# Optimization experiments

Hardware: AMD Instinct MI355X
Metric: run time of the kernel (lower is better)

Reference implementation:

```python
import jax, jax.numpy as jnp
import numpy as np

N_NODES = 100000
N_EDGES = 300000
N_GRAPHS = 2048
F_ATOM = 40
D_IN = 128    # GINInputSize
D_HID = 256   # GINHiddenSize
D_OUT = 512   # FPSize
D_TASK = 1    # OutputSize


def _glorot(key, shape):
    fan_in, fan_out = shape[0], shape[1]
    lim = (6.0 / (fan_in + fan_out)) ** 0.5
    return jax.random.uniform(key, shape, jnp.float32, -lim, lim)


def setup_inputs() -> dict:
    key = jax.random.key(0)
    ks = jax.random.split(key, 16)
    inp = {
        'x': jax.random.normal(ks[0], (N_NODES, F_ATOM), jnp.float32),
        'edge_index': jax.random.randint(ks[1], (2, N_EDGES), 0, N_NODES, jnp.int64),
        'batch': jnp.sort(jax.random.randint(ks[2], (N_NODES,), 0, N_GRAPHS, jnp.int64)),
        # NodeFeatEmbed: MLP([F_ATOM, D_IN]) == single Linear (plain_last)
        'W_embed': _glorot(ks[3], (F_ATOM, D_IN)),
        'b_embed': jnp.zeros((D_IN,), jnp.float32),
        # GINConv eps per layer (train_eps=False -> 0.0 constants)
        'eps': jnp.zeros((3,), jnp.float32),
        # layer 0: MLP([D_IN, D_HID, D_HID])
        'W1_0': _glorot(ks[4], (D_IN, D_HID)),  'b1_0': jnp.zeros((D_HID,), jnp.float32),
        'W2_0': _glorot(ks[5], (D_HID, D_HID)), 'b2_0': jnp.zeros((D_HID,), jnp.float32),
        # layer 1: MLP([D_HID, D_HID, D_HID])
        'W1_1': _glorot(ks[6], (D_HID, D_HID)), 'b1_1': jnp.zeros((D_HID,), jnp.float32),
        'W2_1': _glorot(ks[7], (D_HID, D_HID)), 'b2_1': jnp.zeros((D_HID,), jnp.float32),
        # layer 2 (last, maps to out_channels=FPSize): MLP([D_HID, D_OUT, D_OUT])
        'W1_2': _glorot(ks[8], (D_HID, D_OUT)), 'b1_2': jnp.zeros((D_OUT,), jnp.float32),
        'W2_2': _glorot(ks[9], (D_OUT, D_OUT)), 'b2_2': jnp.zeros((D_OUT,), jnp.float32),
        # task head
        'W_task': _glorot(ks[10], (D_OUT, D_TASK)),
        'b_task': jnp.zeros((D_TASK,), jnp.float32),
    }
    return inp


def _gin_forward(x, edge_index, batch, W_embed, b_embed, eps, layers, W_task, b_task):
    src, dst = edge_index[0], edge_index[1]
    # NodeFeatEmbed
    h = x @ W_embed + b_embed                                    # [N, D_IN]
    n_layers = len(layers)
    for l, (W1, b1, W2, b2) in enumerate(layers):
        # GINConv: MLP((1+eps)*h + sum_{j->i} h_j)
        agg = jax.ops.segment_sum(h[src], dst, num_segments=N_NODES)
        z = (1.0 + eps[l]) * h + agg
        h = jax.nn.relu(z @ W1 + b1) @ W2 + b2
        if l < n_layers - 1:                                     # inter-layer act (not after last)
            h = jax.nn.relu(h)
    # global_add_pool readout
    pooled = jax.ops.segment_sum(h, batch, num_segments=N_GRAPHS)  # [G, D_OUT]
    return pooled @ W_task + b_task                               # [G, D_TASK]


def reference(x, edge_index, batch, W_embed, b_embed, eps,
              W1_0, b1_0, W2_0, b2_0,
              W1_1, b1_1, W2_1, b2_1,
              W1_2, b1_2, W2_2, b2_2,
              W_task, b_task):
    layers = [(W1_0, b1_0, W2_0, b2_0), (W1_1, b1_1, W2_1, b2_1), (W1_2, b1_2, W2_2, b2_2)]
    return _gin_forward(x, edge_index, batch, W_embed, b_embed, eps, layers, W_task, b_task)
```

## Files before the change

### kernel.cpp

```cpp
#include <hip/hip_runtime.h>

#define N_NODES 100000
#define E_EDGES 300000
#define N_GRAPHS 2048

typedef float  floatx4 __attribute__((ext_vector_type(4)));
typedef short  shortx8 __attribute__((ext_vector_type(8)));

__device__ __forceinline__ float bf2f(unsigned short u) {
  return __uint_as_float(((unsigned int)u) << 16);
}
__device__ __forceinline__ unsigned short f2bf(float f) {
  unsigned int u = __float_as_uint(f);
  u += 0x7FFFu + ((u >> 16) & 1u);
  return (unsigned short)(u >> 16);
}

__device__ __forceinline__ void cp16(const void* g, void* l) {
  __builtin_amdgcn_global_load_lds(
      (const __attribute__((address_space(1))) unsigned int*)g,
      (__attribute__((address_space(3))) unsigned int*)l, 16, 0, 0);
}

struct WtJobs {
  const float* W[4];
  unsigned short* Wt[4];
  int K[4];
  int N[4];
};

__global__ __launch_bounds__(256)
void wt4_kernel(WtJobs j) {
  __shared__ unsigned short tile[32][33];
  const int z = blockIdx.z;
  const int K = j.K[z], N = j.N[z];
  const int kb = blockIdx.x * 32, nb = blockIdx.y * 32;
  if (kb >= K || nb >= N) return;
  const float* W = j.W[z];
  unsigned short* Wt = j.Wt[z];
  const int tx = threadIdx.x & 31, ty = threadIdx.x >> 5;
  for (int r = ty; r < 32; r += 8)
    tile[r][tx] = f2bf(W[(size_t)(kb + r) * N + nb + tx]);
  __syncthreads();
  for (int r = ty; r < 32; r += 8)
    Wt[(size_t)(nb + r) * K + kb + tx] = tile[tx][r];
}

__global__ __launch_bounds__(256)
void wf_kernel(const float* __restrict__ We, const float* __restrict__ be,
               const float* __restrict__ W1, unsigned short* __restrict__ WfT) {
  const int n = threadIdx.x;
  const int k = blockIdx.x;
  if (k < 40) {
    float s = 0.f;
    for (int j = 0; j < 128; j++) s = fmaf(We[k * 128 + j], W1[(size_t)j * 256 + n], s);
    WfT[n * 64 + k] = f2bf(s);
  } else {
    float s = 0.f;
    for (int j = 0; j < 128; j++) s = fmaf(be[j], W1[(size_t)j * 256 + n], s);
    WfT[n * 64 + 40] = f2bf(s);
    for (int kk = 41; kk < 64; kk++) WfT[n * 64 + kk] = 0;
  }
}

__global__ __launch_bounds__(256)
void w2v_kernel(const float* __restrict__ W2, const float* __restrict__ b2,
                const float* __restrict__ wt, float* __restrict__ w2v,
                float* __restrict__ c2) {
  const int lane = threadIdx.x & 63;
  const int wave = threadIdx.x >> 6;
  if (blockIdx.x < 128) {
    const int k = blockIdx.x * 4 + wave;
    const float* row = W2 + (size_t)k * 512 + lane * 8;
    float4 a0 = *(const float4*)(row);
    float4 a1 = *(const float4*)(row + 4);
    float4 w0 = *(const float4*)(wt + lane * 8);
    float4 w1 = *(const float4*)(wt + lane * 8 + 4);
    float s = a0.x * w0.x + a0.y * w0.y + a0.z * w0.z + a0.w * w0.w +
              a1.x * w1.x + a1.y * w1.y + a1.z * w1.z + a1.w * w1.w;
#pragma unroll
    for (int off = 32; off > 0; off >>= 1) s += __shfl_down(s, off);
    if (lane == 0) w2v[k] = s;
  } else if (wave == 0) {
    float4 a0 = *(const float4*)(b2 + lane * 8);
    float4 a1 = *(const float4*)(b2 + lane * 8 + 4);
    float4 w0 = *(const float4*)(wt + lane * 8);
    float4 w1 = *(const float4*)(wt + lane * 8 + 4);
    float s = a0.x * w0.x + a0.y * w0.y + a0.z * w0.z + a0.w * w0.w +
              a1.x * w1.x + a1.y * w1.y + a1.z * w1.z + a1.w * w1.w;
#pragma unroll
    for (int off = 32; off > 0; off >>= 1) s += __shfl_down(s, off);
    if (lane == 0) *c2 = s;
  }
}

__global__ __launch_bounds__(256)
void init_nd_kernel(float* __restrict__ nd, const float* __restrict__ c2) {
  int i = blockIdx.x * 256 + threadIdx.x;
  if (i < N_NODES) nd[i] = *c2;
}

__global__ __launch_bounds__(256)
void zero_kernel(int* __restrict__ p, int n) {
  int i = blockIdx.x * 256 + threadIdx.x;
  if (i < n) p[i] = 0;
}

__global__ __launch_bounds__(256)
void hist_kernel(const int* __restrict__ ei, int* __restrict__ deg) {
  int e = blockIdx.x * 256 + threadIdx.x;
  if (e < E_EDGES) atomicAdd(&deg[ei[E_EDGES + e]], 1);
}

__global__ __launch_bounds__(256)
void scan_blk_kernel(const int* __restrict__ in, int* __restrict__ out,
                     int* __restrict__ blk_sums, int n_in, int n_out) {
  __shared__ int sm[256];
  const int t = threadIdx.x;
  const int base = blockIdx.x * 1024 + t * 4;
  int d0 = (base + 0 < n_in) ? in[base + 0] : 0;
  int d1 = (base + 1 < n_in) ? in[base + 1] : 0;
  int d2 = (base + 2 < n_in) ? in[base + 2] : 0;
  int d3 = (base + 3 < n_in) ? in[base + 3] : 0;
  int s = d0 + d1 + d2 + d3;
  sm[t] = s;
  __syncthreads();
  for (int off = 1; off < 256; off <<= 1) {
    int v = (t >= off) ? sm[t - off] : 0;
    __syncthreads();
    sm[t] += v;
    __syncthreads();
  }
  int excl = sm[t] - s;
  if (base + 0 < n_out) out[base + 0] = excl;
  if (base + 1 < n_out) out[base + 1] = excl + d0;
  if (base + 2 < n_out) out[base + 2] = excl + d0 + d1;
  if (base + 3 < n_out) out[base + 3] = excl + d0 + d1 + d2;
  if (t == 255 && blk_sums) blk_sums[blockIdx.x] = sm[255];
}

__global__ __launch_bounds__(256)
void scan_fix_kernel(int* __restrict__ row_ptr, const int* __restrict__ blk_off,
                     int* __restrict__ cursor) {
  int i = blockIdx.x * 256 + threadIdx.x;
  if (i <= N_NODES) {
    int v = row_ptr[i] + blk_off[i >> 10];
    row_ptr[i] = v;
    if (i < N_NODES) cursor[i] = v;
  }
}

__global__ __launch_bounds__(256)
void fill_kernel(const int* __restrict__ ei, int* __restrict__ cursor,
                 int* __restrict__ csr_src) {
  int e = blockIdx.x * 256 + threadIdx.x;
  if (e < E_EDGES) {
    int d = ei[E_EDGES + e];
    int slot = atomicAdd(&cursor[d], 1);
    csr_src[slot] = ei[e];
  }
}

__global__ __launch_bounds__(256)
void gatherx_kernel(const float* __restrict__ X, unsigned short* __restrict__ G,
                    const int* __restrict__ row_ptr, const int* __restrict__ csr,
                    const float* __restrict__ eps) {
  const int node = blockIdx.x * 4 + (threadIdx.x >> 6);
  const int lane = threadIdx.x & 63;
  const float sc = 1.0f + eps[0];
  const int e0 = row_ptr[node];
  const int e1 = row_ptr[node + 1];
  float acc = 0.f;
  if (lane < 40) {
    acc = sc * X[(size_t)node * 40 + lane];
    int e = e0;
    for (; e + 4 <= e1; e += 4) {
      int s0 = csr[e], s1 = csr[e + 1], s2 = csr[e + 2], s3 = csr[e + 3];
      float a0 = X[(size_t)s0 * 40 + lane];
      float a1 = X[(size_t)s1 * 40 + lane];
      float a2 = X[(size_t)s2 * 40 + lane];
      float a3 = X[(size_t)s3 * 40 + lane];
      acc += (a0 + a1) + (a2 + a3);
    }
    for (; e < e1; e++)
      acc += X[(size_t)csr[e] * 40 + lane];
  } else if (lane == 40) {
    acc = sc + (float)(e1 - e0);
  }
  G[(size_t)node * 64 + lane] = f2bf(acc);
}

__global__ __launch_bounds__(256)
void gather_kernel(const unsigned short* __restrict__ H, unsigned short* __restrict__ Z,
                   const int* __restrict__ row_ptr, const int* __restrict__ csr,
                   const float* __restrict__ eps, int l) {
  const int node = blockIdx.x * 4 + (threadIdx.x >> 6);
  const int lane = threadIdx.x & 63;
  const float sc = 1.0f + eps[l];
  uint2 hv = *(const uint2*)(H + (size_t)node * 256 + lane * 4);
  float acc[4];
  acc[0] = sc * bf2f((unsigned short)(hv.x & 0xFFFF));
  acc[1] = sc * bf2f((unsigned short)(hv.x >> 16));
  acc[2] = sc * bf2f((unsigned short)(hv.y & 0xFFFF));
  acc[3] = sc * bf2f((unsigned short)(hv.y >> 16));
  const int e0 = row_ptr[node];
  const int e1 = row_ptr[node + 1];
  int e = e0;
  for (; e + 4 <= e1; e += 4) {
    int s0 = csr[e], s1 = csr[e + 1], s2 = csr[e + 2], s3 = csr[e + 3];
    uint2 a = *(const uint2*)(H + (size_t)s0 * 256 + lane * 4);
    uint2 b = *(const uint2*)(H + (size_t)s1 * 256 + lane * 4);
    uint2 c = *(const uint2*)(H + (size_t)s2 * 256 + lane * 4);
    uint2 d = *(const uint2*)(H + (size_t)s3 * 256 + lane * 4);
    acc[0] += (bf2f((unsigned short)(a.x & 0xFFFF)) + bf2f((unsigned short)(b.x & 0xFFFF))) +
              (bf2f((unsigned short)(c.x & 0xFFFF)) + bf2f((unsigned short)(d.x & 0xFFFF)));
    acc[1] += (bf2f((unsigned short)(a.x >> 16)) + bf2f((unsigned short)(b.x >> 16))) +
              (bf2f((unsigned short)(c.x >> 16)) + bf2f((unsigned short)(d.x >> 16)));
    acc[2] += (bf2f((unsigned short)(a.y & 0xFFFF)) + bf2f((unsigned short)(b.y & 0xFFFF))) +
              (bf2f((unsigned short)(c.y & 0xFFFF)) + bf2f((unsigned short)(d.y & 0xFFFF)));
    acc[3] += (bf2f((unsigned short)(a.y >> 16)) + bf2f((unsigned short)(b.y >> 16))) +
              (bf2f((unsigned short)(c.y >> 16)) + bf2f((unsigned short)(d.y >> 16)));
  }
  for (; e < e1; e++) {
    int s0 = csr[e];
    uint2 a = *(const uint2*)(H + (size_t)s0 * 256 + lane * 4);
    acc[0] += bf2f((unsigned short)(a.x & 0xFFFF));
    acc[1] += bf2f((unsigned short)(a.x >> 16));
    acc[2] += bf2f((unsigned short)(a.y & 0xFFFF));
    acc[3] += bf2f((unsigned short)(a.y >> 16));
  }
  unsigned short z[4] = {f2bf(acc[0]), f2bf(acc[1]), f2bf(acc[2]), f2bf(acc[3])};
  *(uint2*)(Z + (size_t)node * 256 + lane * 4) = *(uint2*)z;
}

template <int K, int NXL, int MODE>
__global__ __launch_bounds__(256, 4)
void gemm_kernel(const unsigned short* __restrict__ A,
                 const unsigned short* __restrict__ Bt,
                 const float* __restrict__ bias, unsigned short* __restrict__ C,
                 const float* __restrict__ w2v, float* __restrict__ nodedot,
                 int M, int N) {
  const int g = blockIdx.x;
  const int mblk = ((g >> (3 + NXL)) << 3) | (g & 7);
  const int nblk = (g >> 3) & ((1 << NXL) - 1);
  const int m0 = mblk * 128;
  const int n0 = nblk * 128;
  if (m0 >= M) return;

  __shared__ unsigned short smem[2 * 128 * 64];
  unsigned short* As = smem;
  unsigned short* Bs = smem + 128 * 64;
  const int tid = threadIdx.x;
  const int lane = tid & 63;
  const int wave = tid >> 6;
  const int wm = (wave & 1) * 64;
  const int wn = (wave >> 1) * 64;
  const int fr = lane & 15;
  const int fq = lane >> 4;

  floatx4 acc[4][4];
#pragma unroll
  for (int i = 0; i < 4; i++)
#pragma unroll
    for (int j = 0; j < 4; j++) acc[i][j] = (floatx4){0.f, 0.f, 0.f, 0.f};

  const unsigned short* gA[4];
  const unsigned short* gB[4];
  unsigned short* lA[4];
  unsigned short* lB[4];
#pragma unroll
  for (int p = 0; p < 4; p++) {
    int c = p * 256 + wave * 64 + lane;
    int row = c >> 3;
    int q = (c & 7) ^ (row & 7);
    int grA = m0 + row;
    if (grA >= M) grA = M - 1;
    gA[p] = A + (size_t)grA * K + q * 8;
    gB[p] = Bt + (size_t)(n0 + row) * K + q * 8;
    lA[p] = &As[(p * 256 + wave * 64) * 8];
    lB[p] = &Bs[(p * 256 + wave * 64) * 8];
  }

  for (int k0 = 0; k0 < K; k0 += 64) {
#pragma unroll
    for (int p = 0; p < 4; p++) cp16(gA[p] + k0, lA[p]);
#pragma unroll
    for (int p = 0; p < 4; p++) cp16(gB[p] + k0, lB[p]);
    __syncthreads();
#pragma unroll
    for (int s0 = 0; s0 < 2; s0++) {
      shortx8 af[4], bf[4];
#pragma unroll
      for (int i = 0; i < 4; i++)
        af[i] = *(const shortx8*)&As[(wm + i * 16 + fr) * 64 +
                                     (((s0 * 4 + fq) ^ (fr & 7)) * 8)];
#pragma unroll
      for (int j = 0; j < 4; j++)
        bf[j] = *(const shortx8*)&Bs[(wn + j * 16 + fr) * 64 +
                                     (((s0 * 4 + fq) ^ (fr & 7)) * 8)];
#pragma unroll
      for (int i = 0; i < 4; i++)
#pragma unroll
        for (int j = 0; j < 4; j++)
          acc[i][j] = __builtin_amdgcn_mfma_f32_16x16x32_bf16(af[i], bf[j], acc[i][j], 0, 0, 0);
    }
    __syncthreads();
  }

  if (MODE == 3) {
    float wv[4], bj[4];
#pragma unroll
    for (int j = 0; j < 4; j++) {
      int col = n0 + wn + j * 16 + fr;
      wv[j] = w2v[col];
      bj[j] = bias[col];
    }
#pragma unroll
    for (int i = 0; i < 4; i++) {
#pragma unroll
      for (int r = 0; r < 4; r++) {
        float p = 0.f;
#pragma unroll
        for (int j = 0; j < 4; j++) p += fmaxf(acc[i][j][r] + bj[j], 0.f) * wv[j];
#pragma unroll
        for (int off = 1; off < 16; off <<= 1) p += __shfl_xor(p, off);
        if (fr == 0) {
          int row = m0 + wm + i * 16 + fq * 4 + r;
          if (row < M) unsafeAtomicAdd(&nodedot[row], p);
        }
      }
    }
  } else {
    unsigned short* Cs = smem;
#pragma unroll
    for (int j = 0; j < 4; j++) {
      int col = wn + j * 16 + fr;
      float bj = bias[n0 + col];
#pragma unroll
      for (int i = 0; i < 4; i++) {
#pragma unroll
        for (int r = 0; r < 4; r++) {
          int row = wm + i * 16 + fq * 4 + r;
          Cs[row * 128 + col] = f2bf(fmaxf(acc[i][j][r] + bj, 0.f));
        }
      }
    }
    __syncthreads();
    const int rcol = (tid & 15) * 8;
#pragma unroll
    for (int p = 0; p < 8; p++) {
      int row = p * 16 + (tid >> 4);
      int grow = m0 + row;
      if (grow < M) {
        uint4 v = *(const uint4*)&Cs[row * 128 + rcol];
        *(uint4*)&C[(size_t)grow * N + n0 + rcol] = v;
      }
    }
  }
}

__global__ __launch_bounds__(256)
void init_out_kernel(float* __restrict__ out, const float* __restrict__ b_task) {
  int g = blockIdx.x * 256 + threadIdx.x;
  if (g < N_GRAPHS) out[g] = b_task[0];
}

__global__ __launch_bounds__(256)
void pool_kernel(const float* __restrict__ nodedot, const int* __restrict__ batch,
                 float* __restrict__ out) {
  int t = blockIdx.x * 256 + threadIdx.x;
  int i0 = t * 64;
  if (i0 >= N_NODES) return;
  int i1 = i0 + 64;
  if (i1 > N_NODES) i1 = N_NODES;
  int g = batch[i0];
  float s = 0.f;
  for (int i = i0; i < i1; i++) {
    int gi = batch[i];
    if (gi != g) { unsafeAtomicAdd(&out[g], s); g = gi; s = 0.f; }
    s += nodedot[i];
  }
  unsafeAtomicAdd(&out[g], s);
}

extern "C" void kernel_launch(void* const* d_in, const int* in_sizes, int n_in,
                              void* d_out, int out_size, void* d_ws, size_t ws_size,
                              hipStream_t stream) {
  const float* x       = (const float*)d_in[0];
  const int*   ei      = (const int*)d_in[1];
  const int*   batch   = (const int*)d_in[2];
  const float* W_embed = (const float*)d_in[3];
  const float* b_embed = (const float*)d_in[4];
  const float* eps     = (const float*)d_in[5];
  const float* W1[3] = {(const float*)d_in[6],  (const float*)d_in[10], (const float*)d_in[14]};
  const float* B1[3] = {(const float*)d_in[7],  (const float*)d_in[11], (const float*)d_in[15]};
  const float* W2[3] = {(const float*)d_in[8],  (const float*)d_in[12], (const float*)d_in[16]};
  const float* B2[3] = {(const float*)d_in[9],  (const float*)d_in[13], (const float*)d_in[17]};
  const float* W_task = (const float*)d_in[18];
  const float* b_task = (const float*)d_in[19];
  float* out = (float*)d_out;

  const size_t OFF_RB  = 51200000;
  const size_t OFF_RZ  = 102400000;
  const size_t OFF_AUX = 153600000;
  if (ws_size < OFF_AUX + 4000000) return;
  unsigned short* RH = (unsigned short*)d_ws;
  unsigned short* RB = (unsigned short*)((char*)d_ws + OFF_RB);
  unsigned short* RZ = (unsigned short*)((char*)d_ws + OFF_RZ);
  char* aux = (char*)d_ws + OFF_AUX;
  int* row_ptr  = (int*)(aux);
  int* cursor   = (int*)(aux + 400016);
  int* csr_src  = (int*)(aux + 800016);
  int* blk_sums = (int*)(aux + 2000016);
  int* blk_off  = (int*)(aux + 2000416);
  float* nodedot = (float*)(aux + 2000816);
  unsigned short* WT = (unsigned short*)(aux + 2400832);
  float* w2v = (float*)(aux + 3200832);
  float* c2  = (float*)(aux + 3202880);
  unsigned short* WfT    = WT;
  unsigned short* Wt2_0  = WT + 32768;
  unsigned short* Wt1_1  = WT + 98304;
  unsigned short* Wt2_1  = WT + 163840;
  unsigned short* Wt1_2  = WT + 229376;

  WtJobs jobs;
  jobs.W[0] = W2[0]; jobs.Wt[0] = Wt2_0; jobs.K[0] = 256; jobs.N[0] = 256;
  jobs.W[1] = W1[1]; jobs.Wt[1] = Wt1_1; jobs.K[1] = 256; jobs.N[1] = 256;
  jobs.W[2] = W2[1]; jobs.Wt[2] = Wt2_1; jobs.K[2] = 256; jobs.N[2] = 256;
  jobs.W[3] = W1[2]; jobs.Wt[3] = Wt1_2; jobs.K[3] = 256; jobs.N[3] = 512;
  wt4_kernel<<<dim3(8, 16, 4), 256, 0, stream>>>(jobs);

  wf_kernel<<<41, 256, 0, stream>>>(W_embed, b_embed, W1[0], WfT);
  w2v_kernel<<<129, 256, 0, stream>>>(W2[2], B2[2], W_task, w2v, c2);

  zero_kernel<<<(N_NODES + 255) / 256, 256, 0, stream>>>(cursor, N_NODES);
  hist_kernel<<<(E_EDGES + 255) / 256, 256, 0, stream>>>(ei, cursor);
  scan_blk_kernel<<<98, 256, 0, stream>>>(cursor, row_ptr, blk_sums, N_NODES, N_NODES + 1);
  scan_blk_kernel<<<1, 256, 0, stream>>>(blk_sums, blk_off, nullptr, 98, 98);
  scan_fix_kernel<<<(N_NODES + 256) / 256, 256, 0, stream>>>(row_ptr, blk_off, cursor);
  fill_kernel<<<(E_EDGES + 255) / 256, 256, 0, stream>>>(ei, cursor, csr_src);

  init_nd_kernel<<<(N_NODES + 255) / 256, 256, 0, stream>>>(nodedot, c2);

  const int MB = (N_NODES + 127) / 128;
  const int MB8 = ((MB + 7) / 8) * 8;

  gatherx_kernel<<<N_NODES / 4, 256, 0, stream>>>(x, RZ, row_ptr, csr_src, eps);
  gemm_kernel<64, 1, 0><<<2 * MB8, 256, 0, stream>>>(RZ, WfT, B1[0], RB, nullptr, nullptr, N_NODES, 256);
  gemm_kernel<256, 1, 0><<<2 * MB8, 256, 0, stream>>>(RB, Wt2_0, B2[0], RH, nullptr, nullptr, N_NODES, 256);

  gather_kernel<<<N_NODES / 4, 256, 0, stream>>>(RH, RZ, row_ptr, csr_src, eps, 1);
  gemm_kernel<256, 1, 0><<<2 * MB8, 256, 0, stream>>>(RZ, Wt1_1, B1[1], RB, nullptr, nullptr, N_NODES, 256);
  gemm_kernel<256, 1, 0><<<2 * MB8, 256, 0, stream>>>(RB, Wt2_1, B2[1], RH, nullptr, nullptr, N_NODES, 256);

  gather_kernel<<<N_NODES / 4, 256, 0, stream>>>(RH, RZ, row_ptr, csr_src, eps, 2);
  gemm_kernel<256, 2, 3><<<4 * MB8, 256, 0, stream>>>(RZ, Wt1_2, B1[2], nullptr, w2v, nodedot, N_NODES, 512);

  init_out_kernel<<<(N_GRAPHS + 255) / 256, 256, 0, stream>>>(out, b_task);
  pool_kernel<<<((N_NODES + 63) / 64 + 255) / 256, 256, 0, stream>>>(nodedot, batch, out);
}
```

Before: 456.1 us.

## Merge prep kernels into one launch and split gather rows across two waves

Folds the weight transpose, fused embed weight, w2v/c2 projection, nodedot zeroing and output bias init into a single prep kernel. The constant c2 is now added per node inside the pool loop, so nodedot no longer has to be initialised from c2. The gather kernel now uses two waves per node, each handling 128 columns with 4-byte loads, which doubles wave count. The aim is fewer kernel launches and more memory-level parallelism in the gather, at the cost of narrower loads and reading the row indices twice.

```diff
diff --git a/kernel.cpp b/kernel.cpp
--- a/kernel.cpp
+++ b/kernel.cpp
@@ -22,82 +22,93 @@
       (__attribute__((address_space(3))) unsigned int*)l, 16, 0, 0);
 }
 
-struct WtJobs {
+struct PrepArgs {
   const float* W[4];
   unsigned short* Wt[4];
   int K[4];
   int N[4];
+  const float* We;
+  const float* be;
+  const float* W1_0;
+  unsigned short* WfT;
+  const float* W2_2;
+  const float* b2_2;
+  const float* wtask;
+  float* w2v;
+  float* c2;
+  float* nodedot;
+  float* out;
+  const float* b_task;
 };
 
 __global__ __launch_bounds__(256)
-void wt4_kernel(WtJobs j) {
-  __shared__ unsigned short tile[32][33];
-  const int z = blockIdx.z;
-  const int K = j.K[z], N = j.N[z];
-  const int kb = blockIdx.x * 32, nb = blockIdx.y * 32;
-  if (kb >= K || nb >= N) return;
-  const float* W = j.W[z];
-  unsigned short* Wt = j.Wt[z];
-  const int tx = threadIdx.x & 31, ty = threadIdx.x >> 5;
-  for (int r = ty; r < 32; r += 8)
-    tile[r][tx] = f2bf(W[(size_t)(kb + r) * N + nb + tx]);
-  __syncthreads();
-  for (int r = ty; r < 32; r += 8)
-    Wt[(size_t)(nb + r) * K + kb + tx] = tile[tx][r];
-}
-
-__global__ __launch_bounds__(256)
-void wf_kernel(const float* __restrict__ We, const float* __restrict__ be,
-               const float* __restrict__ W1, unsigned short* __restrict__ WfT) {
-  const int n = threadIdx.x;
-  const int k = blockIdx.x;
-  if (k < 40) {
-    float s = 0.f;
-    for (int j = 0; j < 128; j++) s = fmaf(We[k * 128 + j], W1[(size_t)j * 256 + n], s);
-    WfT[n * 64 + k] = f2bf(s);
+void prep_kernel(PrepArgs a) {
+  const int blk = blockIdx.x;
+  if (blk < 320) {
+    int z, b;
+    if (blk < 64)       { z = 0; b = blk; }
+    else if (blk < 128) { z = 1; b = blk - 64; }
+    else if (blk < 192) { z = 2; b = blk - 128; }
+    else                { z = 3; b = blk - 192; }
+    const int K = a.K[z], N = a.N[z];
+    const int nt = N / 32;
+    const int kb = (b / nt) * 32, nb = (b % nt) * 32;
+    __shared__ unsigned short tile[32][33];
+    const float* W = a.W[z];
+    unsigned short* Wt = a.Wt[z];
+    const int tx = threadIdx.x & 31, ty = threadIdx.x >> 5;
+    for (int r = ty; r < 32; r += 8)
+      tile[r][tx] = f2bf(W[(size_t)(kb + r) * N + nb + tx]);
+    __syncthreads();
+    for (int r = ty; r < 32; r += 8)
+      Wt[(size_t)(nb + r) * K + kb + tx] = tile[tx][r];
+  } else if (blk < 361) {
+    const int k = blk - 320;
+    const int n = threadIdx.x;
+    if (k < 40) {
+      float s = 0.f;
+      for (int j = 0; j < 128; j++) s = fmaf(a.We[k * 128 + j], a.W1_0[(size_t)j * 256 + n], s);
+      a.WfT[n * 64 + k] = f2bf(s);
+    } else {
+      float s = 0.f;
+      for (int j = 0; j < 128; j++) s = fmaf(a.be[j], a.W1_0[(size_t)j * 256 + n], s);
+      a.WfT[n * 64 + 40] = f2bf(s);
+      for (int kk = 41; kk < 64; kk++) a.WfT[n * 64 + kk] = 0;
+    }
+  } else if (blk < 490) {
+    const int p = blk - 361;
+    const int lane = threadIdx.x & 63;
+    const int wave = threadIdx.x >> 6;
+    if (p < 128) {
+      const int k = p * 4 + wave;
+      const float* row = a.W2_2 + (size_t)k * 512 + lane * 8;
+      float4 a0 = *(const float4*)(row);
+      float4 a1 = *(const float4*)(row + 4);
+      float4 w0 = *(const float4*)(a.wtask + lane * 8);
+      float4 w1 = *(const float4*)(a.wtask + lane * 8 + 4);
+      float s = a0.x * w0.x + a0.y * w0.y + a0.z * w0.z + a0.w * w0.w +
+                a1.x * w1.x + a1.y * w1.y + a1.z * w1.z + a1.w * w1.w;
+#pragma unroll
+      for (int off = 32; off > 0; off >>= 1) s += __shfl_down(s, off);
+      if (lane == 0) a.w2v[k] = s;
+    } else if (wave == 0) {
+      float4 a0 = *(const float4*)(a.b2_2 + lane * 8);
+      float4 a1 = *(const float4*)(a.b2_2 + lane * 8 + 4);
+      float4 w0 = *(const float4*)(a.wtask + lane * 8);
+      float4 w1 = *(const float4*)(a.wtask + lane * 8 + 4);
+      float s = a0.x * w0.x + a0.y * w0.y + a0.z * w0.z + a0.w * w0.w +
+                a1.x * w1.x + a1.y * w1.y + a1.z * w1.z + a1.w * w1.w;
+#pragma unroll
+      for (int off = 32; off > 0; off >>= 1) s += __shfl_down(s, off);
+      if (lane == 0) *a.c2 = s;
+    }
+  } else if (blk < 881) {
+    int i = (blk - 490) * 256 + threadIdx.x;
+    if (i < N_NODES) a.nodedot[i] = 0.f;
   } else {
-    float s = 0.f;
-    for (int j = 0; j < 128; j++) s = fmaf(be[j], W1[(size_t)j * 256 + n], s);
-    WfT[n * 64 + 40] = f2bf(s);
-    for (int kk = 41; kk < 64; kk++) WfT[n * 64 + kk] = 0;
-  }
-}
-
-__global__ __launch_bounds__(256)
-void w2v_kernel(const float* __restrict__ W2, const float* __restrict__ b2,
-                const float* __restrict__ wt, float* __restrict__ w2v,
-                float* __restrict__ c2) {
-  const int lane = threadIdx.x & 63;
-  const int wave = threadIdx.x >> 6;
-  if (blockIdx.x < 128) {
-    const int k = blockIdx.x * 4 + wave;
-    const float* row = W2 + (size_t)k * 512 + lane * 8;
-    float4 a0 = *(const float4*)(row);
-    float4 a1 = *(const float4*)(row + 4);
-    float4 w0 = *(const float4*)(wt + lane * 8);
-    float4 w1 = *(const float4*)(wt + lane * 8 + 4);
-    float s = a0.x * w0.x + a0.y * w0.y + a0.z * w0.z + a0.w * w0.w +
-              a1.x * w1.x + a1.y * w1.y + a1.z * w1.z + a1.w * w1.w;
-#pragma unroll
-    for (int off = 32; off > 0; off >>= 1) s += __shfl_down(s, off);
-    if (lane == 0) w2v[k] = s;
-  } else if (wave == 0) {
-    float4 a0 = *(const float4*)(b2 + lane * 8);
-    float4 a1 = *(const float4*)(b2 + lane * 8 + 4);
-    float4 w0 = *(const float4*)(wt + lane * 8);
-    float4 w1 = *(const float4*)(wt + lane * 8 + 4);
-    float s = a0.x * w0.x + a0.y * w0.y + a0.z * w0.z + a0.w * w0.w +
-              a1.x * w1.x + a1.y * w1.y + a1.z * w1.z + a1.w * w1.w;
-#pragma unroll
-    for (int off = 32; off > 0; off >>= 1) s += __shfl_down(s, off);
-    if (lane == 0) *c2 = s;
-  }
-}
-
-__global__ __launch_bounds__(256)
-void init_nd_kernel(float* __restrict__ nd, const float* __restrict__ c2) {
-  int i = blockIdx.x * 256 + threadIdx.x;
-  if (i < N_NODES) nd[i] = *c2;
+    int g = (blk - 881) * 256 + threadIdx.x;
+    if (g < N_GRAPHS) a.out[g] = a.b_task[0];
+  }
 }
 
 __global__ __launch_bounds__(256)
@@ -194,43 +205,36 @@
 void gather_kernel(const unsigned short* __restrict__ H, unsigned short* __restrict__ Z,
                    const int* __restrict__ row_ptr, const int* __restrict__ csr,
                    const float* __restrict__ eps, int l) {
-  const int node = blockIdx.x * 4 + (threadIdx.x >> 6);
+  const int w = blockIdx.x * 4 + (threadIdx.x >> 6);
+  const int node = w >> 1;
+  const int half = w & 1;
   const int lane = threadIdx.x & 63;
+  const int col = half * 128 + lane * 2;
   const float sc = 1.0f + eps[l];
-  uint2 hv = *(const uint2*)(H + (size_t)node * 256 + lane * 4);
-  float acc[4];
-  acc[0] = sc * bf2f((unsigned short)(hv.x & 0xFFFF));
-  acc[1] = sc * bf2f((unsigned short)(hv.x >> 16));
-  acc[2] = sc * bf2f((unsigned short)(hv.y & 0xFFFF));
-  acc[3] = sc * bf2f((unsigned short)(hv.y >> 16));
+  unsigned int hv = *(const unsigned int*)(H + (size_t)node * 256 + col);
+  float acc0 = sc * bf2f((unsigned short)(hv & 0xFFFF));
+  float acc1 = sc * bf2f((unsigned short)(hv >> 16));
   const int e0 = row_ptr[node];
   const int e1 = row_ptr[node + 1];
   int e = e0;
   for (; e + 4 <= e1; e += 4) {
     int s0 = csr[e], s1 = csr[e + 1], s2 = csr[e + 2], s3 = csr[e + 3];
-    uint2 a = *(const uint2*)(H + (size_t)s0 * 256 + lane * 4);
-    uint2 b = *(const uint2*)(H + (size_t)s1 * 256 + lane * 4);
-    uint2 c = *(const uint2*)(H + (size_t)s2 * 256 + lane * 4);
-    uint2 d = *(const uint2*)(H + (size_t)s3 * 256 + lane * 4);
-    acc[0] += (bf2f((unsigned short)(a.x & 0xFFFF)) + bf2f((unsigned short)(b.x & 0xFFFF))) +
-              (bf2f((unsigned short)(c.x & 0xFFFF)) + bf2f((unsigned short)(d.x & 0xFFFF)));
-    acc[1] += (bf2f((unsigned short)(a.x >> 16)) + bf2f((unsigned short)(b.x >> 16))) +
-              (bf2f((unsigned short)(c.x >> 16)) + bf2f((unsigned short)(d.x >> 16)));
-    acc[2] += (bf2f((unsigned short)(a.y & 0xFFFF)) + bf2f((unsigned short)(b.y & 0xFFFF))) +
-              (bf2f((unsigned short)(c.y & 0xFFFF)) + bf2f((unsigned short)(d.y & 0xFFFF)));
-    acc[3] += (bf2f((unsigned short)(a.y >> 16)) + bf2f((unsigned short)(b.y >> 16))) +
-              (bf2f((unsigned short)(c.y >> 16)) + bf2f((unsigned short)(d.y >> 16)));
+    unsigned int a = *(const unsigned int*)(H + (size_t)s0 * 256 + col);
+    unsigned int b = *(const unsigned int*)(H + (size_t)s1 * 256 + col);
+    unsigned int c = *(const unsigned int*)(H + (size_t)s2 * 256 + col);
+    unsigned int d = *(const unsigned int*)(H + (size_t)s3 * 256 + col);
+    acc0 += (bf2f((unsigned short)(a & 0xFFFF)) + bf2f((unsigned short)(b & 0xFFFF))) +
+            (bf2f((unsigned short)(c & 0xFFFF)) + bf2f((unsigned short)(d & 0xFFFF)));
+    acc1 += (bf2f((unsigned short)(a >> 16)) + bf2f((unsigned short)(b >> 16))) +
+            (bf2f((unsigned short)(c >> 16)) + bf2f((unsigned short)(d >> 16)));
   }
   for (; e < e1; e++) {
-    int s0 = csr[e];
-    uint2 a = *(const uint2*)(H + (size_t)s0 * 256 + lane * 4);
-    acc[0] += bf2f((unsigned short)(a.x & 0xFFFF));
-    acc[1] += bf2f((unsigned short)(a.x >> 16));
-    acc[2] += bf2f((unsigned short)(a.y & 0xFFFF));
-    acc[3] += bf2f((unsigned short)(a.y >> 16));
-  }
-  unsigned short z[4] = {f2bf(acc[0]), f2bf(acc[1]), f2bf(acc[2]), f2bf(acc[3])};
-  *(uint2*)(Z + (size_t)node * 256 + lane * 4) = *(uint2*)z;
+    unsigned int a = *(const unsigned int*)(H + (size_t)csr[e] * 256 + col);
+    acc0 += bf2f((unsigned short)(a & 0xFFFF));
+    acc1 += bf2f((unsigned short)(a >> 16));
+  }
+  unsigned short z[2] = {f2bf(acc0), f2bf(acc1)};
+  *(unsigned int*)(Z + (size_t)node * 256 + col) = *(unsigned int*)z;
 }
 
 template <int K, int NXL, int MODE>
@@ -360,25 +364,20 @@
 }
 
 __global__ __launch_bounds__(256)
-void init_out_kernel(float* __restrict__ out, const float* __restrict__ b_task) {
-  int g = blockIdx.x * 256 + threadIdx.x;
-  if (g < N_GRAPHS) out[g] = b_task[0];
-}
-
-__global__ __launch_bounds__(256)
 void pool_kernel(const float* __restrict__ nodedot, const int* __restrict__ batch,
-                 float* __restrict__ out) {
+                 float* __restrict__ out, const float* __restrict__ c2p) {
   int t = blockIdx.x * 256 + threadIdx.x;
   int i0 = t * 64;
   if (i0 >= N_NODES) return;
   int i1 = i0 + 64;
   if (i1 > N_NODES) i1 = N_NODES;
+  const float c2 = *c2p;
   int g = batch[i0];
   float s = 0.f;
   for (int i = i0; i < i1; i++) {
     int gi = batch[i];
     if (gi != g) { unsafeAtomicAdd(&out[g], s); g = gi; s = 0.f; }
-    s += nodedot[i];
+    s += nodedot[i] + c2;
   }
   unsafeAtomicAdd(&out[g], s);
 }
@@ -423,15 +422,15 @@
   unsigned short* Wt2_1  = WT + 163840;
   unsigned short* Wt1_2  = WT + 229376;
 
-  WtJobs jobs;
-  jobs.W[0] = W2[0]; jobs.Wt[0] = Wt2_0; jobs.K[0] = 256; jobs.N[0] = 256;
-  jobs.W[1] = W1[1]; jobs.Wt[1] = Wt1_1; jobs.K[1] = 256; jobs.N[1] = 256;
-  jobs.W[2] = W2[1]; jobs.Wt[2] = Wt2_1; jobs.K[2] = 256; jobs.N[2] = 256;
-  jobs.W[3] = W1[2]; jobs.Wt[3] = Wt1_2; jobs.K[3] = 256; jobs.N[3] = 512;
-  wt4_kernel<<<dim3(8, 16, 4), 256, 0, stream>>>(jobs);
-
-  wf_kernel<<<41, 256, 0, stream>>>(W_embed, b_embed, W1[0], WfT);
-  w2v_kernel<<<129, 256, 0, stream>>>(W2[2], B2[2], W_task, w2v, c2);
+  PrepArgs pa;
+  pa.W[0] = W2[0]; pa.Wt[0] = Wt2_0; pa.K[0] = 256; pa.N[0] = 256;
+  pa.W[1] = W1[1]; pa.Wt[1] = Wt1_1; pa.K[1] = 256; pa.N[1] = 256;
+  pa.W[2] = W2[1]; pa.Wt[2] = Wt2_1; pa.K[2] = 256; pa.N[2] = 256;
+  pa.W[3] = W1[2]; pa.Wt[3] = Wt1_2; pa.K[3] = 256; pa.N[3] = 512;
+  pa.We = W_embed; pa.be = b_embed; pa.W1_0 = W1[0]; pa.WfT = WfT;
+  pa.W2_2 = W2[2]; pa.b2_2 = B2[2]; pa.wtask = W_task; pa.w2v = w2v; pa.c2 = c2;
+  pa.nodedot = nodedot; pa.out = out; pa.b_task = b_task;
+  prep_kernel<<<889, 256, 0, stream>>>(pa);
 
   zero_kernel<<<(N_NODES + 255) / 256, 256, 0, stream>>>(cursor, N_NODES);
   hist_kernel<<<(E_EDGES + 255) / 256, 256, 0, stream>>>(ei, cursor);
@@ -440,8 +439,6 @@
   scan_fix_kernel<<<(N_NODES + 256) / 256, 256, 0, stream>>>(row_ptr, blk_off, cursor);
   fill_kernel<<<(E_EDGES + 255) / 256, 256, 0, stream>>>(ei, cursor, csr_src);
 
-  init_nd_kernel<<<(N_NODES + 255) / 256, 256, 0, stream>>>(nodedot, c2);
-
   const int MB = (N_NODES + 127) / 128;
   const int MB8 = ((MB + 7) / 8) * 8;
 
@@ -449,13 +446,12 @@
   gemm_kernel<64, 1, 0><<<2 * MB8, 256, 0, stream>>>(RZ, WfT, B1[0], RB, nullptr, nullptr, N_NODES, 256);
   gemm_kernel<256, 1, 0><<<2 * MB8, 256, 0, stream>>>(RB, Wt2_0, B2[0], RH, nullptr, nullptr, N_NODES, 256);
 
-  gather_kernel<<<N_NODES / 4, 256, 0, stream>>>(RH, RZ, row_ptr, csr_src, eps, 1);
+  gather_kernel<<<N_NODES / 2, 256, 0, stream>>>(RH, RZ, row_ptr, csr_src, eps, 1);
   gemm_kernel<256, 1, 0><<<2 * MB8, 256, 0, stream>>>(RZ, Wt1_1, B1[1], RB, nullptr, nullptr, N_NODES, 256);
   gemm_kernel<256, 1, 0><<<2 * MB8, 256, 0, stream>>>(RB, Wt2_1, B2[1], RH, nullptr, nullptr, N_NODES, 256);
 
-  gather_kernel<<<N_NODES / 4, 256, 0, stream>>>(RH, RZ, row_ptr, csr_src, eps, 2);
+  gather_kernel<<<N_NODES / 2, 256, 0, stream>>>(RH, RZ, row_ptr, csr_src, eps, 2);
   gemm_kernel<256, 2, 3><<<4 * MB8, 256, 0, stream>>>(RZ, Wt1_2, B1[2], nullptr, w2v, nodedot, N_NODES, 512);
 
-  init_out_kernel<<<(N_GRAPHS + 255) / 256, 256, 0, stream>>>(out, b_task);
-  pool_kernel<<<((N_NODES + 63) / 64 + 255) / 256, 256, 0, stream>>>(nodedot, batch, out);
-}
+  pool_kernel<<<((N_NODES + 63) / 64 + 255) / 256, 256, 0, stream>>>(nodedot, batch, out, c2);
+}
```

After: 475.7 us. +4.3%, slower.
